# Performance work log

Hardware: AMD Instinct MI355X
Metric: run time of the kernel (lower is better)

Reference implementation:

```python
import jax, jax.numpy as jnp
import numpy as np

NB, B, IN, HID = 8, 256, 512, 512
G = 4 * HID
WB, IB, ABNM = 8, 8, 8
NL = 0.05


def quant(x, bits, r):
    # QuantFunc.forward: scale, clamp to (-1+1/step, 1-1/step), round to step grid, rescale
    step = 2.0 ** (bits - 1)
    x01 = jnp.clip(x / r, -1.0 + 1.0 / step, 1.0 - 1.0 / step)
    return jnp.round(x01 * step) / step * r


def pact(x, a):
    # pact_a_bmm vectorized over the block dim: sign(x)*0.5*(|x| - ||x|-a| + a)
    a3 = a[:, None, None]
    return jnp.sign(x) * 0.5 * (jnp.abs(x) - jnp.abs(jnp.abs(x) - a3) + a3)


def custom_mm(inp, w, b, nw, nb):
    # CustomMM_bmm.forward: quantize weights/bias (range 1.0), add scaled noise, bmm
    wq = quant(w, WB, 1.0)
    bq = quant(b, WB, 1.0)
    out = jnp.einsum('bni,bio->bno', inp, wq + nw * jnp.max(w) * NL)
    return out + bq + nb * jnp.max(b) * NL


def setup_inputs():
    key = jax.random.key(0)
    ks = jax.random.split(key, 11)
    inp = {
        'input': jax.random.normal(ks[0], (B, IN), jnp.float32),
        'hx': jax.random.normal(ks[1], (NB, B, HID), jnp.float32),
        'cx': jax.random.normal(ks[2], (NB, B, HID), jnp.float32),
        'weight_ih': jax.random.normal(ks[3], (NB, IN, G), jnp.float32),
        'weight_hh': jax.random.normal(ks[4], (NB, HID, G), jnp.float32),
        'bias_ih': jax.random.normal(ks[5], (NB, 1, G), jnp.float32),
        'bias_hh': jax.random.normal(ks[6], (NB, 1, G), jnp.float32),
        'noise_wih': jax.random.normal(ks[7], (NB, IN, G), jnp.float32),
        'noise_whh': jax.random.normal(ks[8], (NB, HID, G), jnp.float32),
        'noise_bih': jax.random.normal(ks[9], (NB, 1, G), jnp.float32),
        'noise_bhh': jax.random.normal(ks[10], (NB, 1, G), jnp.float32),
        'a1': jnp.full((NB,), 128.0, jnp.float32),
        'a3': jnp.ones((NB,), jnp.float32),
        'a4': jnp.ones((NB,), jnp.float32),
        'a5': jnp.ones((NB,), jnp.float32),
        'a6': jnp.ones((NB,), jnp.float32),
        'a7': jnp.full((NB,), 4.0, jnp.float32),
        'a8': jnp.ones((NB,), jnp.float32),
        'a9': jnp.full((NB,), 4.0, jnp.float32),
        'a10': jnp.ones((NB,), jnp.float32),
        'a11': jnp.full((NB,), 4.0, jnp.float32),
    }
    return inp


def reference(input, hx, cx, weight_ih, weight_hh, bias_ih, bias_hh,
              noise_wih, noise_whh, noise_bih, noise_bhh,
              a1, a3, a4, a5, a6, a7, a8, a9, a10, a11):
    xr = jnp.broadcast_to(input[None], (NB,) + input.shape)  # input.repeat(n_blocks,1,1)
    xq = quant(pact(xr, a1), IB, a1[:, None, None])
    gates = custom_mm(xq, weight_ih, bias_ih, noise_wih, noise_bih) \
          + custom_mm(hx, weight_hh, bias_hh, noise_whh, noise_bhh)
    i, j, f, o = jnp.split(gates, 4, axis=2)
    qp = lambda x, a: quant(pact(x, a), ABNM, a[:, None, None])
    fg = qp(jax.nn.sigmoid(f), a3)
    ig = qp(jax.nn.sigmoid(i), a4)
    act = qp(jnp.tanh(j), a5)
    og = qp(jax.nn.sigmoid(o), a6)
    gated = qp(cx * fg, a7)
    actin = qp(ig * act, a8)
    new_c = qp(gated + actin, a9)
    actc = qp(jnp.tanh(new_c), a10)
    new_h = qp(actc * og, a11)
    return new_h, new_c
```

## Files before the change

kernel.cpp:

```cpp
#include <hip/hip_runtime.h>
#include <hip/hip_bf16.h>

#define NBATCH 8
#define BROWS 256
#define KDIM 512
#define HIDD 512
#define GDIM 2048
#define KSTEP 64
#define NIT (KDIM / KSTEP)

typedef float f32x4 __attribute__((ext_vector_type(4)));
typedef __bf16 bf16x8 __attribute__((ext_vector_type(8)));

__device__ __forceinline__ unsigned fenc(float f) {
    unsigned u = __float_as_uint(f);
    return (u & 0x80000000u) ? ~u : (u | 0x80000000u);
}
__device__ __forceinline__ float fdec(unsigned e) {
    unsigned u = (e & 0x80000000u) ? (e & 0x7fffffffu) : ~e;
    return __uint_as_float(u);
}
__device__ __forceinline__ unsigned umaxu(unsigned a, unsigned b) { return a > b ? a : b; }

__device__ __forceinline__ float qpact(float x, float a) {
    float ax = fabsf(x);
    float p  = copysignf(0.5f * (ax - fabsf(ax - a) + a), x);
    float x01 = p / a;
    x01 = fminf(fmaxf(x01, -0.9921875f), 0.9921875f);
    return (rintf(x01 * 128.f) * 0.0078125f) * a;
}
__device__ __forceinline__ float q1(float x) {
    float x01 = fminf(fmaxf(x, -0.9921875f), 0.9921875f);
    return rintf(x01 * 128.f) * 0.0078125f;
}
__device__ __forceinline__ float sigmf(float x) { return 1.0f / (1.0f + expf(-x)); }

__global__ void k_init(unsigned* m) { if (threadIdx.x < 4) m[threadIdx.x] = 0u; }

__global__ void k_max(const float* __restrict__ w_ih, const float* __restrict__ w_hh,
                      const float* __restrict__ b_ih, const float* __restrict__ b_hh,
                      unsigned* __restrict__ omax) {
    int which = blockIdx.y;
    const float* src = which == 0 ? w_ih : which == 1 ? w_hh : which == 2 ? b_ih : b_hh;
    int n4 = (which < 2 ? NBATCH * KDIM * GDIM : NBATCH * GDIM) >> 2;
    unsigned best = 0u;
    int stride = gridDim.x * blockDim.x;
    for (int i = blockIdx.x * blockDim.x + threadIdx.x; i < n4; i += stride) {
        float4 v = ((const float4*)src)[i];
        best = umaxu(best, fenc(v.x)); best = umaxu(best, fenc(v.y));
        best = umaxu(best, fenc(v.z)); best = umaxu(best, fenc(v.w));
    }
    #pragma unroll
    for (int off = 32; off > 0; off >>= 1)
        best = umaxu(best, (unsigned)__shfl_down((int)best, off, 64));
    __shared__ unsigned red[4];
    int lane = threadIdx.x & 63, wv = threadIdx.x >> 6;
    if (lane == 0) red[wv] = best;
    __syncthreads();
    if (threadIdx.x == 0) {
        unsigned b2 = umaxu(umaxu(red[0], red[1]), umaxu(red[2], red[3]));
        atomicMax(&omax[which], b2);
    }
}

__global__ void k_prep(const float* __restrict__ input, const float* __restrict__ hx,
                       const float* __restrict__ bih, const float* __restrict__ bhh,
                       const float* __restrict__ nbih, const float* __restrict__ nbhh,
                       const float* __restrict__ a1, const unsigned* __restrict__ maxes,
                       __hip_bfloat16* __restrict__ xqh, __hip_bfloat16* __restrict__ hxh,
                       __hip_bfloat16* __restrict__ hxl, float* __restrict__ bias_comb) {
    const int NX = NBATCH * BROWS * KDIM;
    const int NH = NBATCH * BROWS * HIDD;
    const int NBC = NBATCH * GDIM;
    int total = NX + NH + NBC;
    int stride = gridDim.x * blockDim.x;
    for (int i = blockIdx.x * blockDim.x + threadIdx.x; i < total; i += stride) {
        if (i < NX) {
            int nb = i >> 17;
            int rem = i & 131071;
            float v = qpact(input[rem], a1[nb]);
            xqh[i] = __float2bfloat16(v);
        } else if (i < NX + NH) {
            int j = i - NX;
            float h = hx[j];
            __hip_bfloat16 hi = __float2bfloat16(h);
            hxh[j] = hi;
            hxl[j] = __float2bfloat16(h - __bfloat162float(hi));
        } else {
            int j = i - NX - NH;
            float mb_ih = fdec(maxes[2]);
            float mb_hh = fdec(maxes[3]);
            bias_comb[j] = q1(bih[j]) + (nbih[j] * mb_ih) * 0.05f
                         + q1(bhh[j]) + (nbhh[j] * mb_hh) * 0.05f;
        }
    }
}

__global__ __launch_bounds__(1024, 1) void k_gemm(
    const float* __restrict__ w_ih, const float* __restrict__ w_hh,
    const float* __restrict__ n_ih, const float* __restrict__ n_hh,
    const __hip_bfloat16* __restrict__ xqh, const __hip_bfloat16* __restrict__ hxh,
    const __hip_bfloat16* __restrict__ hxl,
    const float* __restrict__ bias_comb, const float* __restrict__ cx,
    const float* __restrict__ a3, const float* __restrict__ a4, const float* __restrict__ a5,
    const float* __restrict__ a6, const float* __restrict__ a7, const float* __restrict__ a8,
    const float* __restrict__ a9, const float* __restrict__ a10, const float* __restrict__ a11,
    const unsigned* __restrict__ maxes,
    float* __restrict__ out_h, float* __restrict__ out_c)
{
    __shared__ __hip_bfloat16 Bsm[2][4][64][72];

    int tid = threadIdx.x;
    int lane = tid & 63, wv = tid >> 6;
    int nb = blockIdx.x & 7;
    int cb = blockIdx.x >> 3;

    const float* wih_b = w_ih + nb * KDIM * GDIM;
    const float* whh_b = w_hh + nb * KDIM * GDIM;
    const float* nih_b = n_ih + nb * KDIM * GDIM;
    const float* nhh_b = n_hh + nb * KDIM * GDIM;
    const __hip_bfloat16* xq_b = xqh + nb * BROWS * KDIM;
    const __hip_bfloat16* hh_b = hxh + nb * BROWS * KDIM;
    const __hip_bfloat16* hl_b = hxl + nb * BROWS * KDIM;

    float c_ih = fdec(maxes[0]);
    float c_hh = fdec(maxes[1]);

    f32x4 acc[4] = {};

    int lh = lane & 15;
    int g  = lane >> 4;
    int arow = (wv << 4) + lh;

    int sn   = tid & 63;
    int soct = (tid >> 6) & 7;
    int shh  = tid >> 9;
    const float* wsrc = shh ? whh_b : wih_b;
    const float* zsrc = shh ? nhh_b : nih_b;
    float cmax = shh ? c_hh : c_ih;
    int matHi = shh << 1;
    int scol = ((sn >> 4) << 9) + (cb << 4) + (sn & 15);

    float rwa[8], rza[8], rwb[8], rzb[8];
    bf16x8 ax0, ax1, ah0, ah1, al0, al1;

#define STAGE(RW, RZ, K0) {                                  \
    int kb = (K0) + (soct << 3);                             \
    _Pragma("unroll")                                        \
    for (int j = 0; j < 8; ++j) {                            \
        int gx = (kb + j) * GDIM + scol;                     \
        RW[j] = wsrc[gx]; RZ[j] = zsrc[gx];                  \
    } }

#define ALOAD(K0) {                                          \
    int a0 = arow * KDIM + (K0) + (g << 3);                  \
    ax0 = *(const bf16x8*)(xq_b + a0);                       \
    ax1 = *(const bf16x8*)(xq_b + a0 + 32);                  \
    ah0 = *(const bf16x8*)(hh_b + a0);                       \
    ah1 = *(const bf16x8*)(hh_b + a0 + 32);                  \
    al0 = *(const bf16x8*)(hl_b + a0);                       \
    al1 = *(const bf16x8*)(hl_b + a0 + 32);                  \
    asm volatile("" :: "v"(__builtin_bit_cast(f32x4, ax0)), "v"(__builtin_bit_cast(f32x4, ax1)), \
                       "v"(__builtin_bit_cast(f32x4, ah0)), "v"(__builtin_bit_cast(f32x4, ah1)), \
                       "v"(__builtin_bit_cast(f32x4, al0)), "v"(__builtin_bit_cast(f32x4, al1))); }

#define CVT(P, RW, RZ) {                                     \
    bf16x8 hi8, lo8;                                         \
    _Pragma("unroll")                                        \
    for (int j = 0; j < 8; ++j) {                            \
        float w = RW[j];                                     \
        float wq = rintf(fminf(fmaxf(w, -0.9921875f), 0.9921875f) * 128.f) * 0.0078125f; \
        float e = wq + (RZ[j] * cmax) * 0.05f;               \
        __hip_bfloat16 h = __float2bfloat16(e);              \
        float lo = e - __bfloat162float(h);                  \
        __hip_bfloat16 l = __float2bfloat16(lo);             \
        hi8[j] = *reinterpret_cast<__bf16*>(&h);             \
        lo8[j] = *reinterpret_cast<__bf16*>(&l);             \
    }                                                        \
    *(bf16x8*)&Bsm[P][matHi][sn][soct << 3] = hi8;           \
    *(bf16x8*)&Bsm[P][matHi + 1][sn][soct << 3] = lo8; }

#define COMPUTE(P) {                                         \
    _Pragma("unroll")                                        \
    for (int nf = 0; nf < 4; ++nf) {                         \
        int n = (nf << 4) + lh;                              \
        int kb0 = g << 3, kb1 = 32 + kb0;                    \
        bf16x8 b0 = *(const bf16x8*)&Bsm[P][0][n][kb0];      \
        bf16x8 b1 = *(const bf16x8*)&Bsm[P][1][n][kb0];      \
        bf16x8 b2 = *(const bf16x8*)&Bsm[P][2][n][kb0];      \
        bf16x8 b3 = *(const bf16x8*)&Bsm[P][3][n][kb0];      \
        acc[nf] = __builtin_amdgcn_mfma_f32_16x16x32_bf16(ax0, b0, acc[nf], 0, 0, 0); \
        acc[nf] = __builtin_amdgcn_mfma_f32_16x16x32_bf16(ax0, b1, acc[nf], 0, 0, 0); \
        acc[nf] = __builtin_amdgcn_mfma_f32_16x16x32_bf16(ah0, b2, acc[nf], 0, 0, 0); \
        acc[nf] = __builtin_amdgcn_mfma_f32_16x16x32_bf16(ah0, b3, acc[nf], 0, 0, 0); \
        acc[nf] = __builtin_amdgcn_mfma_f32_16x16x32_bf16(al0, b2, acc[nf], 0, 0, 0); \
        b0 = *(const bf16x8*)&Bsm[P][0][n][kb1];             \
        b1 = *(const bf16x8*)&Bsm[P][1][n][kb1];             \
        b2 = *(const bf16x8*)&Bsm[P][2][n][kb1];             \
        b3 = *(const bf16x8*)&Bsm[P][3][n][kb1];             \
        acc[nf] = __builtin_amdgcn_mfma_f32_16x16x32_bf16(ax1, b0, acc[nf], 0, 0, 0); \
        acc[nf] = __builtin_amdgcn_mfma_f32_16x16x32_bf16(ax1, b1, acc[nf], 0, 0, 0); \
        acc[nf] = __builtin_amdgcn_mfma_f32_16x16x32_bf16(ah1, b2, acc[nf], 0, 0, 0); \
        acc[nf] = __builtin_amdgcn_mfma_f32_16x16x32_bf16(ah1, b3, acc[nf], 0, 0, 0); \
        acc[nf] = __builtin_amdgcn_mfma_f32_16x16x32_bf16(al1, b2, acc[nf], 0, 0, 0); \
    } }

    STAGE(rwa, rza, 0);
    STAGE(rwb, rzb, KSTEP);

    for (int it = 0; it < NIT; it += 2) {
        ALOAD(it * KSTEP);
        CVT(0, rwa, rza);
        if (it + 2 < NIT) STAGE(rwa, rza, (it + 2) * KSTEP);
        __syncthreads();
        COMPUTE(0);
        ALOAD((it + 1) * KSTEP);
        CVT(1, rwb, rzb);
        if (it + 3 < NIT) STAGE(rwb, rzb, (it + 3) * KSTEP);
        __syncthreads();
        COMPUTE(1);
    }

    int hcol = (cb << 4) + lh;
    float A3 = a3[nb], A4 = a4[nb], A5 = a5[nb], A6 = a6[nb], A7 = a7[nb];
    float A8 = a8[nb], A9 = a9[nb], A10 = a10[nb], A11 = a11[nb];
    float bc_i = bias_comb[nb * GDIM + hcol];
    float bc_j = bias_comb[nb * GDIM + 512 + hcol];
    float bc_f = bias_comb[nb * GDIM + 1024 + hcol];
    float bc_o = bias_comb[nb * GDIM + 1536 + hcol];
    #pragma unroll
    for (int rg = 0; rg < 4; ++rg) {
        int r = (wv << 4) + (g << 2) + rg;
        float gi = acc[0][rg] + bc_i;
        float gj = acc[1][rg] + bc_j;
        float gf = acc[2][rg] + bc_f;
        float go = acc[3][rg] + bc_o;
        float fg = qpact(sigmf(gf), A3);
        float ig = qpact(sigmf(gi), A4);
        float act = qpact(tanhf(gj), A5);
        float og = qpact(sigmf(go), A6);
        int oidx = (nb * BROWS + r) * HIDD + hcol;
        float cv = cx[oidx];
        float gated = qpact(cv * fg, A7);
        float actin = qpact(ig * act, A8);
        float ncv = qpact(gated + actin, A9);
        float acv = qpact(tanhf(ncv), A10);
        float nhv = qpact(acv * og, A11);
        out_h[oidx] = nhv;
        out_c[oidx] = ncv;
    }
}

extern "C" void kernel_launch(void* const* d_in, const int* in_sizes, int n_in,
                              void* d_out, int out_size, void* d_ws, size_t ws_size,
                              hipStream_t stream) {
    const float* input = (const float*)d_in[0];
    const float* hx    = (const float*)d_in[1];
    const float* cx    = (const float*)d_in[2];
    const float* w_ih  = (const float*)d_in[3];
    const float* w_hh  = (const float*)d_in[4];
    const float* b_ih  = (const float*)d_in[5];
    const float* b_hh  = (const float*)d_in[6];
    const float* n_wih = (const float*)d_in[7];
    const float* n_whh = (const float*)d_in[8];
    const float* n_bih = (const float*)d_in[9];
    const float* n_bhh = (const float*)d_in[10];
    const float* a1  = (const float*)d_in[11];
    const float* a3  = (const float*)d_in[12];
    const float* a4  = (const float*)d_in[13];
    const float* a5  = (const float*)d_in[14];
    const float* a6  = (const float*)d_in[15];
    const float* a7  = (const float*)d_in[16];
    const float* a8  = (const float*)d_in[17];
    const float* a9  = (const float*)d_in[18];
    const float* a10 = (const float*)d_in[19];
    const float* a11 = (const float*)d_in[20];

    float* out_h = (float*)d_out;
    float* out_c = out_h + NBATCH * BROWS * HIDD;

    char* ws = (char*)d_ws;
    unsigned* maxes = (unsigned*)ws;
    __hip_bfloat16* xqh = (__hip_bfloat16*)(ws + 256);
    __hip_bfloat16* hxh = (__hip_bfloat16*)(ws + 256 + 2097152);
    __hip_bfloat16* hxl = (__hip_bfloat16*)(ws + 256 + 2 * 2097152);
    float* bias_comb    = (float*)(ws + 256 + 3 * 2097152);

    k_init<<<1, 64, 0, stream>>>(maxes);
    k_max<<<dim3(256, 4), 256, 0, stream>>>(w_ih, w_hh, b_ih, b_hh, maxes);
    k_prep<<<2048, 256, 0, stream>>>(input, hx, b_ih, b_hh, n_bih, n_bhh, a1, maxes,
                                     xqh, hxh, hxl, bias_comb);
    k_gemm<<<NBATCH * 32, 1024, 0, stream>>>(w_ih, w_hh, n_wih, n_whh, xqh, hxh, hxl,
                                             bias_comb, cx,
                                             a3, a4, a5, a6, a7, a8, a9, a10, a11,
                                             maxes, out_h, out_c);
}
```

Before: 85.49 us.

## Split LSTM cell epilogue out of GEMM into separate vectorized kernel

The GEMM kernel now covers 64 contiguous gate columns per block, so each staged weight column is contiguous instead of gathered from four gate groups. It writes raw gates plus bias to a workspace buffer. A new elementwise kernel then applies the quantized LSTM cell with float4 loads and stores. The init kernel is replaced by a memset, and the register-pinning asm barrier in the A-load is removed. The aim is more coalesced weight staging and a lighter GEMM epilogue, at the cost of an extra kernel launch and a round trip of the gate tensor through global memory.

```diff
diff --git a/kernel.cpp b/kernel.cpp
--- a/kernel.cpp
+++ b/kernel.cpp
@@ -34,8 +34,6 @@
     return rintf(x01 * 128.f) * 0.0078125f;
 }
 __device__ __forceinline__ float sigmf(float x) { return 1.0f / (1.0f + expf(-x)); }
-
-__global__ void k_init(unsigned* m) { if (threadIdx.x < 4) m[threadIdx.x] = 0u; }
 
 __global__ void k_max(const float* __restrict__ w_ih, const float* __restrict__ w_hh,
                       const float* __restrict__ b_ih, const float* __restrict__ b_hh,
@@ -101,19 +99,16 @@
     const float* __restrict__ n_ih, const float* __restrict__ n_hh,
     const __hip_bfloat16* __restrict__ xqh, const __hip_bfloat16* __restrict__ hxh,
     const __hip_bfloat16* __restrict__ hxl,
-    const float* __restrict__ bias_comb, const float* __restrict__ cx,
-    const float* __restrict__ a3, const float* __restrict__ a4, const float* __restrict__ a5,
-    const float* __restrict__ a6, const float* __restrict__ a7, const float* __restrict__ a8,
-    const float* __restrict__ a9, const float* __restrict__ a10, const float* __restrict__ a11,
+    const float* __restrict__ bias_comb,
     const unsigned* __restrict__ maxes,
-    float* __restrict__ out_h, float* __restrict__ out_c)
+    float* __restrict__ gates)
 {
     __shared__ __hip_bfloat16 Bsm[2][4][64][72];
 
     int tid = threadIdx.x;
     int lane = tid & 63, wv = tid >> 6;
     int nb = blockIdx.x & 7;
-    int cb = blockIdx.x >> 3;
+    int gc = blockIdx.x >> 3;
 
     const float* wih_b = w_ih + nb * KDIM * GDIM;
     const float* whh_b = w_hh + nb * KDIM * GDIM;
@@ -139,7 +134,7 @@
     const float* zsrc = shh ? nhh_b : nih_b;
     float cmax = shh ? c_hh : c_ih;
     int matHi = shh << 1;
-    int scol = ((sn >> 4) << 9) + (cb << 4) + (sn & 15);
+    int scol = (gc << 6) + sn;
 
     float rwa[8], rza[8], rwb[8], rzb[8];
     bf16x8 ax0, ax1, ah0, ah1, al0, al1;
@@ -160,9 +155,7 @@
     ah1 = *(const bf16x8*)(hh_b + a0 + 32);                  \
     al0 = *(const bf16x8*)(hl_b + a0);                       \
     al1 = *(const bf16x8*)(hl_b + a0 + 32);                  \
-    asm volatile("" :: "v"(__builtin_bit_cast(f32x4, ax0)), "v"(__builtin_bit_cast(f32x4, ax1)), \
-                       "v"(__builtin_bit_cast(f32x4, ah0)), "v"(__builtin_bit_cast(f32x4, ah1)), \
-                       "v"(__builtin_bit_cast(f32x4, al0)), "v"(__builtin_bit_cast(f32x4, al1))); }
+    }
 
 #define CVT(P, RW, RZ) {                                     \
     bf16x8 hi8, lo8;                                         \
@@ -221,34 +214,57 @@
         COMPUTE(1);
     }
 
-    int hcol = (cb << 4) + lh;
+    #pragma unroll
+    for (int nf = 0; nf < 4; ++nf) {
+        int gcol = (gc << 6) + (nf << 4) + lh;
+        float bc = bias_comb[nb * GDIM + gcol];
+        #pragma unroll
+        for (int rg = 0; rg < 4; ++rg) {
+            int r = (wv << 4) + (g << 2) + rg;
+            gates[((nb * BROWS + r) * GDIM) + gcol] = acc[nf][rg] + bc;
+        }
+    }
+}
+
+__global__ __launch_bounds__(512) void k_cell(
+    const float* __restrict__ gates, const float* __restrict__ cx,
+    const float* __restrict__ a3, const float* __restrict__ a4, const float* __restrict__ a5,
+    const float* __restrict__ a6, const float* __restrict__ a7, const float* __restrict__ a8,
+    const float* __restrict__ a9, const float* __restrict__ a10, const float* __restrict__ a11,
+    float* __restrict__ out_h, float* __restrict__ out_c)
+{
+    int idx = blockIdx.x * blockDim.x + threadIdx.x;
+    int nb = idx >> 15;
+    int rem = idx & 32767;
+    const float* gb = gates + (size_t)(nb * BROWS * GDIM) + rem * 4
+                    - (rem >> 7) * 2048 + (rem >> 7) * 2048;
+    int row = rem >> 7;
+    int hq  = rem & 127;
+    const float* gr = gates + ((size_t)(nb * BROWS + row) * GDIM) + hq * 4;
+    f32x4 gi = *(const f32x4*)(gr);
+    f32x4 gj = *(const f32x4*)(gr + 512);
+    f32x4 gf = *(const f32x4*)(gr + 1024);
+    f32x4 go = *(const f32x4*)(gr + 1536);
+    int oidx = (nb * BROWS + row) * HIDD + hq * 4;
+    f32x4 cv = *(const f32x4*)(cx + oidx);
     float A3 = a3[nb], A4 = a4[nb], A5 = a5[nb], A6 = a6[nb], A7 = a7[nb];
     float A8 = a8[nb], A9 = a9[nb], A10 = a10[nb], A11 = a11[nb];
-    float bc_i = bias_comb[nb * GDIM + hcol];
-    float bc_j = bias_comb[nb * GDIM + 512 + hcol];
-    float bc_f = bias_comb[nb * GDIM + 1024 + hcol];
-    float bc_o = bias_comb[nb * GDIM + 1536 + hcol];
+    f32x4 nh, nc;
     #pragma unroll
-    for (int rg = 0; rg < 4; ++rg) {
-        int r = (wv << 4) + (g << 2) + rg;
-        float gi = acc[0][rg] + bc_i;
-        float gj = acc[1][rg] + bc_j;
-        float gf = acc[2][rg] + bc_f;
-        float go = acc[3][rg] + bc_o;
-        float fg = qpact(sigmf(gf), A3);
-        float ig = qpact(sigmf(gi), A4);
-        float act = qpact(tanhf(gj), A5);
-        float og = qpact(sigmf(go), A6);
-        int oidx = (nb * BROWS + r) * HIDD + hcol;
-        float cv = cx[oidx];
-        float gated = qpact(cv * fg, A7);
+    for (int j = 0; j < 4; ++j) {
+        float fg = qpact(sigmf(gf[j]), A3);
+        float ig = qpact(sigmf(gi[j]), A4);
+        float act = qpact(tanhf(gj[j]), A5);
+        float og = qpact(sigmf(go[j]), A6);
+        float gated = qpact(cv[j] * fg, A7);
         float actin = qpact(ig * act, A8);
         float ncv = qpact(gated + actin, A9);
         float acv = qpact(tanhf(ncv), A10);
-        float nhv = qpact(acv * og, A11);
-        out_h[oidx] = nhv;
-        out_c[oidx] = ncv;
-    }
+        nh[j] = qpact(acv * og, A11);
+        nc[j] = ncv;
+    }
+    *(f32x4*)(out_h + oidx) = nh;
+    *(f32x4*)(out_c + oidx) = nc;
 }
 
 extern "C" void kernel_launch(void* const* d_in, const int* in_sizes, int n_in,
@@ -285,13 +301,14 @@
     __hip_bfloat16* hxh = (__hip_bfloat16*)(ws + 256 + 2097152);
     __hip_bfloat16* hxl = (__hip_bfloat16*)(ws + 256 + 2 * 2097152);
     float* bias_comb    = (float*)(ws + 256 + 3 * 2097152);
-
-    k_init<<<1, 64, 0, stream>>>(maxes);
+    float* gates        = (float*)(ws + 256 + 3 * 2097152 + 65536);
+
+    hipMemsetAsync(maxes, 0, 32, stream);
     k_max<<<dim3(256, 4), 256, 0, stream>>>(w_ih, w_hh, b_ih, b_hh, maxes);
     k_prep<<<2048, 256, 0, stream>>>(input, hx, b_ih, b_hh, n_bih, n_bhh, a1, maxes,
                                      xqh, hxh, hxl, bias_comb);
     k_gemm<<<NBATCH * 32, 1024, 0, stream>>>(w_ih, w_hh, n_wih, n_whh, xqh, hxh, hxl,
-                                             bias_comb, cx,
-                                             a3, a4, a5, a6, a7, a8, a9, a10, a11,
-                                             maxes, out_h, out_c);
-}
+                                             bias_comb, maxes, gates);
+    k_cell<<<512, 512, 0, stream>>>(gates, cx, a3, a4, a5, a6, a7, a8, a9, a10, a11,
+                                    out_h, out_c);
+}
```

Result: faster. 83.29 us (-2.6%).
